# Kernel tuning notes

Hardware: AMD Instinct MI355X
Metric: run time of the kernel (lower is better)

## Reference

```python
import jax, jax.numpy as jnp
import numpy as np

B, C, N, M = 16, 256, 4096, 1024
EPS = 1e-5


def geometry_disentangle(x, num_select):
    # x: [B, C, N]. Variation score = L2 norm of mean-centered feature per point.
    score = jnp.linalg.norm(x - x.mean(axis=2, keepdims=True), axis=1)  # [B, N]
    _, idx_s = jax.lax.top_k(score, num_select)    # sharp: highest variation
    _, idx_g = jax.lax.top_k(-score, num_select)   # gentle: lowest variation
    sharp = jnp.take_along_axis(x, idx_s[:, None, :], axis=2)   # [B, C, M]
    gentle = jnp.take_along_axis(x, idx_g[:, None, :], axis=2)  # [B, C, M]
    return sharp, gentle


def cross_attention(x, ctx, Wq, bq, Wk, bk, Wv, bv, Wo, bo):
    # x: [B, C, N], ctx: [B, M, C] -> [B, C, N]
    c = x.shape[1]
    q = jnp.einsum('bcn,dc->bdn', x, Wq) + bq[None, :, None]  # conv1x1 on x
    k = jnp.einsum('bmc,dc->bmd', ctx, Wk) + bk
    v = jnp.einsum('bmc,dc->bmd', ctx, Wv) + bv
    scores = jnp.einsum('bdn,bmd->bnm', q, k) / jnp.sqrt(jnp.asarray(c, x.dtype))
    attn = jax.nn.softmax(scores, axis=-1)                     # [B, N, M]
    y = jnp.einsum('bnm,bmd->bdn', attn, v)                    # [B, C, N]
    y = jnp.einsum('bdn,ed->ben', y, Wo) + bo[None, :, None]   # output conv1x1
    return x + y


def conv_bn_relu(h, Wf, bf, gamma, beta):
    # Conv1d(k=1) + BatchNorm1d (training-mode batch stats) + ReLU. h: [B, 2C, N]
    y = jnp.einsum('bcn,dc->bdn', h, Wf) + bf[None, :, None]   # [B, C, N]
    mu = y.mean(axis=(0, 2), keepdims=True)
    var = y.var(axis=(0, 2), keepdims=True)
    y = (y - mu) * jax.lax.rsqrt(var + EPS)
    y = y * gamma[None, :, None] + beta[None, :, None]
    return jax.nn.relu(y)


def setup_inputs() -> dict:
    key = jax.random.key(0)
    ks = jax.random.split(key, 20)
    s = 0.02

    def w(k, shape):
        return (jax.random.normal(k, shape, dtype=jnp.float32) * s)

    inp = {
        'x': jax.random.normal(ks[0], (B, C, N), dtype=jnp.float32),
        'num_select': M,
        # sharp attention params
        'Wq_s': w(ks[1], (C, C)), 'bq_s': jnp.zeros((C,), jnp.float32),
        'Wk_s': w(ks[2], (C, C)), 'bk_s': jnp.zeros((C,), jnp.float32),
        'Wv_s': w(ks[3], (C, C)), 'bv_s': jnp.zeros((C,), jnp.float32),
        'Wo_s': w(ks[4], (C, C)), 'bo_s': jnp.zeros((C,), jnp.float32),
        # gentle attention params
        'Wq_g': w(ks[5], (C, C)), 'bq_g': jnp.zeros((C,), jnp.float32),
        'Wk_g': w(ks[6], (C, C)), 'bk_g': jnp.zeros((C,), jnp.float32),
        'Wv_g': w(ks[7], (C, C)), 'bv_g': jnp.zeros((C,), jnp.float32),
        'Wo_g': w(ks[8], (C, C)), 'bo_g': jnp.zeros((C,), jnp.float32),
        # fuse: Conv1d(2C -> C) + BN
        'Wf': w(ks[9], (C, 2 * C)), 'bf': jnp.zeros((C,), jnp.float32),
        'gamma': jnp.ones((C,), jnp.float32), 'beta': jnp.zeros((C,), jnp.float32),
    }
    return inp


def reference(x, Wq_s, bq_s, Wk_s, bk_s, Wv_s, bv_s, Wo_s, bo_s,
              Wq_g, bq_g, Wk_g, bk_g, Wv_g, bv_g, Wo_g, bo_g,
              Wf, bf, gamma, beta, num_select):
    sharp, gentle = geometry_disentangle(x, num_select)
    y_s = cross_attention(x, sharp.transpose(0, 2, 1), Wq_s, bq_s, Wk_s, bk_s, Wv_s, bv_s, Wo_s, bo_s)
    y_g = cross_attention(x, gentle.transpose(0, 2, 1), Wq_g, bq_g, Wk_g, bk_g, Wv_g, bv_g, Wo_g, bo_g)
    h = jnp.concatenate([y_s, y_g], axis=1)  # [B, 2C, N]
    return conv_bn_relu(h, Wf, bf, gamma, beta)
```

## Files before the change

### kernel.cpp

```cpp
#include <hip/hip_runtime.h>

#define BB 16
#define CC 256
#define NN 4096
#define MM 1024
#define EPSV 1e-5f
#define SCALE (1.0f/16.0f)

#define OFF_MU    0
#define OFF_SCORE 4096
#define OFF_IDX   69632
#define OFF_U     102400
#define OFF_WVZ   167936
#define OFF_WF12  233472
#define OFF_BVZ   299008
#define OFF_BZ    299264
#define OFF_W16   299520
#define OFF_XG    430592
#define OFF_K16   2527744
#define OFF_VT16  4624896
#define OFF_Z     6722048
#define OFF_BN    23499264
#define FIXED_F   23499776

typedef __attribute__((ext_vector_type(8))) short s16x8;
typedef __attribute__((ext_vector_type(4))) float f32x4;

__device__ __forceinline__ unsigned short f2bf(float f) {
    unsigned int u = __float_as_uint(f);
    return (unsigned short)((u + 0x7FFFu + ((u >> 16) & 1u)) >> 16);
}
__device__ __forceinline__ float bf2f(unsigned short h) {
    return __uint_as_float(((unsigned int)h) << 16);
}

__global__ __launch_bounds__(256) void zero_bn_kernel(float* bn) {
    int t = threadIdx.x;
    bn[t] = 0.f; bn[t + CC] = 0.f;
}

__global__ __launch_bounds__(256) void zero_rsum_kernel(float* r) {
    r[blockIdx.x * 256 + threadIdx.x] = 0.f;
}

__global__ __launch_bounds__(256) void mean_kernel(const float* __restrict__ x, float* __restrict__ mu) {
    int c = blockIdx.x, b = blockIdx.y, t = threadIdx.x;
    const float4* p = (const float4*)(x + ((size_t)b * CC + c) * NN);
    float s = 0.f;
    for (int n = t; n < NN / 4; n += 256) { float4 v = p[n]; s += (v.x + v.y) + (v.z + v.w); }
    __shared__ float red[256];
    red[t] = s; __syncthreads();
    for (int w = 128; w > 0; w >>= 1) { if (t < w) red[t] += red[t + w]; __syncthreads(); }
    if (t == 0) mu[b * CC + c] = red[0] * (1.0f / NN);
}

__global__ __launch_bounds__(256) void transpose_score_kernel(const float* __restrict__ x,
                                                              const float* __restrict__ mu,
                                                              unsigned short* __restrict__ xT,
                                                              float* __restrict__ score) {
    __shared__ float tile[32][33];
    __shared__ float smu[32];
    int b = blockIdx.z, c0 = blockIdx.y * 32, n0 = blockIdx.x * 32, t = threadIdx.x;
    int nl = t & 31, cr = t >> 5;
    if (t < 32) smu[t] = mu[b * CC + c0 + t];
#pragma unroll
    for (int q = 0; q < 4; ++q)
        tile[cr + q * 8][nl] = x[((size_t)b * CC + c0 + cr + q * 8) * NN + n0 + nl];
    __syncthreads();
    int nr = t >> 3, cq = t & 7;
    uint2 p;
    p.x = (unsigned int)f2bf(tile[cq * 4 + 0][nr]) | ((unsigned int)f2bf(tile[cq * 4 + 1][nr]) << 16);
    p.y = (unsigned int)f2bf(tile[cq * 4 + 2][nr]) | ((unsigned int)f2bf(tile[cq * 4 + 3][nr]) << 16);
    *(uint2*)&xT[((size_t)b * NN + n0 + nr) * CC + c0 + cq * 4] = p;
    int n = t & 31, cseg = t >> 5;
    float part = 0.f;
#pragma unroll
    for (int q = 0; q < 4; ++q) {
        float d = tile[cseg * 4 + q][n] - smu[cseg * 4 + q];
        part += d * d;
    }
    __syncthreads();
    tile[n][cseg] = part;
    __syncthreads();
    if (t < 32) {
        float s = 0.f;
#pragma unroll
        for (int j = 0; j < 8; ++j) s += tile[t][j];
        atomicAdd(&score[(size_t)b * NN + n0 + t], s);
    }
}

__global__ __launch_bounds__(1024) void select_kernel(const float* __restrict__ score,
                                                      int* __restrict__ idx_s, int* __restrict__ idx_g) {
    int b = blockIdx.x, t = threadIdx.x;
    __shared__ unsigned int keys[NN];
    __shared__ unsigned int hist[256];
    __shared__ unsigned int sbin, skrem;
    __shared__ int outcnt, eqcnt;
    __shared__ int eqidx[NN];
    for (int q = t; q < NN; q += 1024) keys[q] = __float_as_uint(score[(size_t)b * NN + q]);
    __syncthreads();
    for (int r = 0; r < 2; ++r) {
        unsigned int flip = r ? 0xFFFFFFFFu : 0u;
        unsigned int prefix = 0u, pmask = 0u;
        unsigned int k = MM;
        for (int pass = 0; pass < 4; ++pass) {
            int shift = 24 - 8 * pass;
            if (t < 256) hist[t] = 0u;
            __syncthreads();
            for (int q = t; q < NN; q += 1024) {
                unsigned int kv = keys[q] ^ flip;
                if ((kv & pmask) == prefix) atomicAdd(&hist[(kv >> shift) & 255u], 1u);
            }
            __syncthreads();
            for (int off = 1; off < 256; off <<= 1) {
                unsigned int v = 0u;
                if (t < 256) v = hist[t] + ((t + off < 256) ? hist[t + off] : 0u);
                __syncthreads();
                if (t < 256) hist[t] = v;
                __syncthreads();
            }
            if (t < 256) {
                unsigned int sj = hist[t], sj1 = (t < 255) ? hist[t + 1] : 0u;
                if (sj >= k && sj1 < k) { sbin = (unsigned int)t; skrem = k - sj1; }
            }
            __syncthreads();
            prefix |= sbin << shift;
            pmask |= 0xFFu << shift;
            k = skrem;
            __syncthreads();
        }
        unsigned int T = prefix;
        unsigned int krem = k;
        int* outp = r ? idx_g : idx_s;
        if (t == 0) { outcnt = 0; eqcnt = 0; }
        __syncthreads();
        for (int q = t; q < NN; q += 1024) {
            unsigned int kv = keys[q] ^ flip;
            if (kv > T) { int pp = atomicAdd(&outcnt, 1); outp[(size_t)b * MM + pp] = q; }
            else if (kv == T) { int pp = atomicAdd(&eqcnt, 1); eqidx[pp] = q; }
        }
        __syncthreads();
        int ne = eqcnt;
        for (int i = t; i < ne; i += 1024) {
            int me = eqidx[i];
            int rank = 0;
            for (int j = 0; j < ne; ++j) rank += (eqidx[j] < me) ? 1 : 0;
            if (rank < (int)krem) { int pp = atomicAdd(&outcnt, 1); outp[(size_t)b * MM + pp] = me; }
        }
        __syncthreads();
    }
}

__global__ __launch_bounds__(256) void bz_kernel(const float* __restrict__ Wf, const float* __restrict__ bf,
                                                 const float* __restrict__ bo_s, const float* __restrict__ bo_g,
                                                 float* __restrict__ bz) {
    int e = threadIdx.x;
    float acc = bf[e];
    for (int c = 0; c < CC; ++c)
        acc += Wf[e * 2 * CC + c] * bo_s[c] + Wf[e * 2 * CC + CC + c] * bo_g[c];
    bz[e] = acc;
}

__global__ __launch_bounds__(256) void wf12_kernel(const float* __restrict__ Wf, float* __restrict__ Wf12) {
    int e = blockIdx.x, c = threadIdx.x;
    Wf12[e * CC + c] = Wf[e * 2 * CC + c] + Wf[e * 2 * CC + CC + c];
}

__global__ __launch_bounds__(256) void prep1_kernel(
    const float* __restrict__ Wo, const float* __restrict__ Wv,
    const float* __restrict__ Wq, const float* __restrict__ Wk,
    const float* __restrict__ bq, const float* __restrict__ bk, const float* __restrict__ bv,
    float* __restrict__ WoWv, unsigned short* __restrict__ W2_16,
    float* __restrict__ wob, float* __restrict__ u, float* __restrict__ b2)
{
    int xr = blockIdx.x, y = blockIdx.y, t = threadIdx.x;
    if (y == 0) {
        __shared__ float arow[CC];
        arow[t] = Wo[xr * CC + t];
        __syncthreads();
        float acc = 0.f;
        for (int k = 0; k < CC; ++k) acc += arow[k] * Wv[k * CC + t];
        WoWv[xr * CC + t] = acc;
    } else if (y == 1) {
        __shared__ float aq[CC];
        aq[t] = Wq[t * CC + xr];
        __syncthreads();
        float acc = 0.f;
        for (int c = 0; c < CC; ++c) acc += aq[c] * Wk[c * CC + t];
        W2_16[xr * CC + t] = f2bf(acc);
    } else if (xr == 0) {
        float a1 = 0.f, a2 = 0.f, a3 = 0.f;
        for (int c = 0; c < CC; ++c) {
            a1 += Wo[t * CC + c] * bv[c];
            a2 += bq[c] * Wk[c * CC + t];
            a3 += Wq[c * CC + t] * bk[c];
        }
        wob[t] = a1; u[t] = a2; b2[t] = a3;
        if (t == 0) { float s = 0.f; for (int c = 0; c < CC; ++c) s += bq[c] * bk[c]; u[CC] = s; }
    }
}

__global__ __launch_bounds__(256) void prep2_kernel(
    const float* __restrict__ Wf, int aoff, const float* __restrict__ WoWv,
    const float* __restrict__ wob, unsigned short* __restrict__ Wvz16, float* __restrict__ bvz)
{
    int e = blockIdx.x, t = threadIdx.x;
    __shared__ float arow[CC];
    __shared__ float red[256];
    arow[t] = Wf[e * 2 * CC + aoff + t];
    __syncthreads();
    float acc = 0.f;
    for (int k = 0; k < CC; ++k) acc += arow[k] * WoWv[k * CC + t];
    Wvz16[e * CC + t] = f2bf(acc);
    red[t] = arow[t] * wob[t];
    __syncthreads();
    for (int w = 128; w > 0; w >>= 1) { if (t < w) red[t] += red[t + w]; __syncthreads(); }
    if (t == 0) bvz[e] = red[0];
}

__global__ __launch_bounds__(256) void beta_kernel(const unsigned short* __restrict__ Xg,
                                                   const float* __restrict__ u, float* __restrict__ beta) {
    int row = blockIdx.x * 4 + (threadIdx.x >> 6);
    int l = threadIdx.x & 63;
    uint2 p = *(const uint2*)&Xg[(size_t)row * CC + l * 4];
    float acc = bf2f((unsigned short)(p.x & 0xFFFF)) * u[l * 4]
              + bf2f((unsigned short)(p.x >> 16)) * u[l * 4 + 1]
              + bf2f((unsigned short)(p.y & 0xFFFF)) * u[l * 4 + 2]
              + bf2f((unsigned short)(p.y >> 16)) * u[l * 4 + 3];
    acc += __shfl_xor(acc, 1); acc += __shfl_xor(acc, 2); acc += __shfl_xor(acc, 4);
    acc += __shfl_xor(acc, 8); acc += __shfl_xor(acc, 16); acc += __shfl_xor(acc, 32);
    if (l == 0) beta[row] = acc + u[CC];
}

__global__ __launch_bounds__(256) void conv_bf16_kernel(const float* __restrict__ src,
                                                        unsigned short* __restrict__ dst) {
    int i = blockIdx.x * 256 + threadIdx.x;
    float4 v = *(const float4*)(src + (size_t)i * 4);
    uint2 p;
    p.x = (unsigned int)f2bf(v.x) | ((unsigned int)f2bf(v.y) << 16);
    p.y = (unsigned int)f2bf(v.z) | ((unsigned int)f2bf(v.w) << 16);
    *(uint2*)&dst[(size_t)i * 4] = p;
}

__global__ __launch_bounds__(256) void gather_kernel(const unsigned short* __restrict__ xT,
                                                     const int* __restrict__ idx,
                                                     unsigned short* __restrict__ Xg) {
    int row = blockIdx.x * 4 + (threadIdx.x >> 6);
    int l = threadIdx.x & 63;
    int b = row >> 10, m = row & (MM - 1);
    int src = idx[b * MM + m];
    *(uint2*)&Xg[(size_t)row * CC + l * 4] =
        *(const uint2*)&xT[((size_t)b * NN + src) * CC + l * 4];
}

template<int OMODE>
__global__ __launch_bounds__(256, 3) void gemm_bt(
    const unsigned short* __restrict__ A, size_t a_bs,
    const unsigned short* __restrict__ Bw, size_t b_bs,
    const float* __restrict__ bias,
    void* __restrict__ outp, size_t o_bs, int ldo)
{
    __shared__ __align__(16) unsigned short As[128 * 32];
    __shared__ __align__(16) unsigned short Bs[128 * 32];
    int z = blockIdx.z;
    const unsigned short* Ab = A + z * a_bs + (size_t)blockIdx.x * 128 * CC;
    const unsigned short* Bb = Bw + z * b_bs + (size_t)blockIdx.y * 128 * CC;
    int t = threadIdx.x, w = t >> 6, l = t & 63, g = l >> 4, c16 = l & 15;
    int wi = w >> 1, wj = w & 1;
    int srow = t >> 2, skq = (t & 3) * 8;

    f32x4 acc[4][4];
#pragma unroll
    for (int a = 0; a < 4; ++a)
#pragma unroll
        for (int bq = 0; bq < 4; ++bq) acc[a][bq] = (f32x4){0.f, 0.f, 0.f, 0.f};

    for (int ks = 0; ks < 8; ++ks) {
        int k0 = ks * 32;
        uint4 a0 = *(const uint4*)(Ab + (size_t)srow * CC + k0 + skq);
        uint4 a1 = *(const uint4*)(Ab + (size_t)(srow + 64) * CC + k0 + skq);
        uint4 b0 = *(const uint4*)(Bb + (size_t)srow * CC + k0 + skq);
        uint4 b1 = *(const uint4*)(Bb + (size_t)(srow + 64) * CC + k0 + skq);
        __syncthreads();
        *(uint4*)&As[srow * 32 + skq] = a0;
        *(uint4*)&As[(srow + 64) * 32 + skq] = a1;
        *(uint4*)&Bs[srow * 32 + skq] = b0;
        *(uint4*)&Bs[(srow + 64) * 32 + skq] = b1;
        __syncthreads();
        s16x8 af[4], bf4[4];
#pragma unroll
        for (int fi = 0; fi < 4; ++fi)
            af[fi] = *(const s16x8*)&As[(wi * 64 + fi * 16 + c16) * 32 + g * 8];
#pragma unroll
        for (int fj = 0; fj < 4; ++fj)
            bf4[fj] = *(const s16x8*)&Bs[(wj * 64 + fj * 16 + c16) * 32 + g * 8];
#pragma unroll
        for (int fi = 0; fi < 4; ++fi)
#pragma unroll
            for (int fj = 0; fj < 4; ++fj)
                acc[fi][fj] = __builtin_amdgcn_mfma_f32_16x16x32_bf16(af[fi], bf4[fj], acc[fi][fj], 0, 0, 0);
    }

    int i0 = blockIdx.x * 128 + wi * 64, j0 = blockIdx.y * 128 + wj * 64;
#pragma unroll
    for (int fi = 0; fi < 4; ++fi) {
#pragma unroll
        for (int fj = 0; fj < 4; ++fj) {
            int colg = j0 + fj * 16 + c16;
#pragma unroll
            for (int r = 0; r < 4; ++r) {
                int rowg = i0 + fi * 16 + g * 4 + r;
                float v = acc[fi][fj][r] + (OMODE == 2 ? bias[rowg] : bias[colg]);
                if (OMODE == 0)
                    ((float*)outp)[z * o_bs + (size_t)rowg * ldo + colg] = v;
                else
                    ((unsigned short*)outp)[z * o_bs + (size_t)rowg * ldo + colg] = f2bf(v);
            }
        }
    }
}

__global__ __attribute__((amdgpu_flat_work_group_size(512, 512)))
__attribute__((amdgpu_waves_per_eu(2, 2)))
void fused_attn(
    const unsigned short* __restrict__ Q,
    const unsigned short* __restrict__ K,
    const unsigned short* __restrict__ Vt,
    const float* __restrict__ beta,
    float* __restrict__ Z)
{
    extern __shared__ __align__(16) unsigned char smem[];
    float* rsl = (float*)(smem + 114688);
    float* bs  = (float*)(smem + 115712);

    int z = blockIdx.z;
    int n0 = blockIdx.x * 128;
    int t = threadIdx.x, w = t >> 6, l = t & 63, g = l >> 4, c16 = l & 15;
    int wn = w >> 1, wc = w & 1;

    const unsigned short* Qb = Q + ((size_t)z * NN + n0) * CC;
    const char* Kzb = (const char*)(K + (size_t)z * MM * CC);
    const char* Vzb = (const char*)(Vt + (size_t)z * CC * MM);

    bs[t] = beta[(size_t)z * MM + t];
    bs[t + 512] = beta[(size_t)z * MM + t + 512];

    s16x8 q[2][8];
#pragma unroll
    for (int fi = 0; fi < 2; ++fi)
#pragma unroll
        for (int ks = 0; ks < 8; ++ks)
            q[fi][ks] = *(const s16x8*)&Qb[(size_t)(wn * 32 + fi * 16 + c16) * CC + ks * 32 + g * 8];

    f32x4 o[2][8];
#pragma unroll
    for (int fi = 0; fi < 2; ++fi)
#pragma unroll
        for (int fj = 0; fj < 8; ++fj) o[fi][fj] = (f32x4){0.f, 0.f, 0.f, 0.f};
    float rs[2][4];
#pragma unroll
    for (int fi = 0; fi < 2; ++fi)
#pragma unroll
        for (int r = 0; r < 4; ++r) rs[fi][r] = 0.f;

    auto issueK = [&](int buf, int m0) {
#pragma unroll
        for (int j = 0; j < 2; ++j) {
            int cid = w * 2 + j;
            int row = cid * 2 + (l >> 5);
            int srcoff = ((l & 31) * 16) ^ ((row & 7) << 4);
            const char* gp = Kzb + (size_t)(m0 + row) * 512 + srcoff;
            __builtin_amdgcn_global_load_lds(
                (const __attribute__((address_space(1))) void*)gp,
                (__attribute__((address_space(3))) void*)(smem + buf * 16384 + cid * 1024),
                16, 0, 0);
        }
    };
    auto issueV = [&](int slot, int m0) {
#pragma unroll
        for (int j = 0; j < 2; ++j) {
            int cid = w * 2 + j;
            int row = cid * 16 + (l >> 2);
            int srcoff = ((l & 3) * 16) ^ (((row >> 1) & 3) << 4);
            const char* gp = Vzb + (size_t)row * 2048 + (size_t)m0 * 2 + srcoff;
            __builtin_amdgcn_global_load_lds(
                (const __attribute__((address_space(1))) void*)gp,
                (__attribute__((address_space(3))) void*)(smem + 32768 + slot * 16384 + cid * 1024),
                16, 0, 0);
        }
    };

    auto qk_exp = [&](int buf, int par, int m0) {
        const unsigned char* Ks = smem + buf * 16384;
        unsigned char* Ps = smem + 81920 + par * 16384;
        f32x4 sacc[2];
#pragma unroll
        for (int fi = 0; fi < 2; ++fi) sacc[fi] = (f32x4){0.f, 0.f, 0.f, 0.f};
        int mr = wc * 16 + c16;
        __builtin_amdgcn_s_setprio(1);
#pragma unroll
        for (int ks = 0; ks < 8; ++ks) {
            s16x8 kf = *(const s16x8*)(Ks + ((mr * 512 + ks * 64 + g * 16) ^ ((mr & 7) << 4)));
#pragma unroll
            for (int fi = 0; fi < 2; ++fi)
                sacc[fi] = __builtin_amdgcn_mfma_f32_16x16x32_bf16(q[fi][ks], kf, sacc[fi], 0, 0, 0);
        }
        __builtin_amdgcn_s_setprio(0);
        float bet = bs[m0 + wc * 16 + c16];
#pragma unroll
        for (int fi = 0; fi < 2; ++fi)
#pragma unroll
            for (int r = 0; r < 4; ++r) {
                float e = __expf((sacc[fi][r] + bet) * SCALE);
                unsigned short h = f2bf(e);
                int nr = wn * 32 + fi * 16 + g * 4 + r;
                *(unsigned short*)(Ps + ((nr * 128 + (wc * 16 + c16) * 2) ^ ((nr & 7) << 4))) = h;
                rs[fi][r] += bf2f(h);
            }
    };
    auto pv = [&](int slot, int par) {
        const unsigned char* Vs = smem + 32768 + slot * 16384;
        const unsigned char* Ps = smem + 81920 + par * 16384;
        s16x8 pa[2];
#pragma unroll
        for (int fi = 0; fi < 2; ++fi) {
            int nr = wn * 32 + fi * 16 + c16;
            pa[fi] = *(const s16x8*)(Ps + ((nr * 128 + g * 16) ^ ((nr & 7) << 4)));
        }
        __builtin_amdgcn_s_setprio(1);
#pragma unroll
        for (int fj = 0; fj < 8; ++fj) {
            int er = wc * 128 + fj * 16 + c16;
            s16x8 vb = *(const s16x8*)(Vs + ((er * 64 + g * 16) ^ (((er >> 1) & 3) << 4)));
#pragma unroll
            for (int fi = 0; fi < 2; ++fi)
                o[fi][fj] = __builtin_amdgcn_mfma_f32_16x16x32_bf16(pa[fi], vb, o[fi][fj], 0, 0, 0);
        }
        __builtin_amdgcn_s_setprio(0);
    };

    issueK(0, 0); issueV(0, 0);
    issueK(1, 32); issueV(1, 32);
    __syncthreads();
    qk_exp(0, 0, 0);

    for (int mt = 0; mt < 32; ++mt) {
        __syncthreads();
        if (mt < 30) {
            issueK(mt & 1, (mt + 2) * 32);
            issueV((mt + 2) % 3, (mt + 2) * 32);
        }
        __builtin_amdgcn_sched_barrier(0);
        if (mt < 31) qk_exp((mt + 1) & 1, (mt + 1) & 1, (mt + 1) * 32);
        pv(mt % 3, mt & 1);
    }

#pragma unroll
    for (int fi = 0; fi < 2; ++fi)
#pragma unroll
        for (int r = 0; r < 4; ++r) {
            float v = rs[fi][r];
            v += __shfl_xor(v, 1); v += __shfl_xor(v, 2);
            v += __shfl_xor(v, 4); v += __shfl_xor(v, 8);
            if (c16 == 0) rsl[wc * 128 + wn * 32 + fi * 16 + g * 4 + r] = v;
        }
    __syncthreads();
    float* Zb = Z + ((size_t)z * NN + n0) * CC;
#pragma unroll
    for (int fi = 0; fi < 2; ++fi)
#pragma unroll
        for (int r = 0; r < 4; ++r) {
            int nr = wn * 32 + fi * 16 + g * 4 + r;
            float inv = 1.0f / (rsl[nr] + rsl[128 + nr]);
#pragma unroll
            for (int fj = 0; fj < 8; ++fj) {
                int e = wc * 128 + fj * 16 + c16;
                Zb[(size_t)nr * CC + e] += o[fi][fj][r] * inv;
            }
        }
}

__global__ __launch_bounds__(256) void bn_stats_kernel(const float* __restrict__ Z, float* __restrict__ bn) {
    int blk = blockIdx.x, e = threadIdx.x;
    const float* p = Z + (size_t)blk * 256 * CC + e;
    float s1 = 0.f, s2 = 0.f;
    for (int r = 0; r < 256; ++r) { float v = p[(size_t)r * CC]; s1 += v; s2 += v * v; }
    atomicAdd(&bn[e], s1);
    atomicAdd(&bn[CC + e], s2);
}

__global__ __launch_bounds__(256) void bn_apply_kernel(const float* __restrict__ Z, const float* __restrict__ bn,
                                                       const float* __restrict__ gamma, const float* __restrict__ beta,
                                                       float* __restrict__ out) {
    int b = blockIdx.z, e0 = blockIdx.y * 32, n0 = blockIdx.x * 32, t = threadIdx.x;
    __shared__ float tile[32][33];
    int c = t & 31, r0 = (t >> 5) * 4;
#pragma unroll
    for (int q = 0; q < 4; ++q)
        tile[r0 + q][c] = Z[((size_t)b * NN + n0 + r0 + q) * CC + e0 + c];
    __syncthreads();
    int n = t & 31, er0 = (t >> 5) * 4;
    const float invcnt = 1.0f / (BB * NN);
#pragma unroll
    for (int q = 0; q < 4; ++q) {
        int e = e0 + er0 + q;
        float mean = bn[e] * invcnt;
        float var = bn[CC + e] * invcnt - mean * mean;
        float rsq = rsqrtf(var + EPSV);
        float v = (tile[n][er0 + q] - mean) * rsq * gamma[e] + beta[e];
        out[((size_t)b * CC + e) * NN + n0 + n] = fmaxf(v, 0.f);
    }
}

extern "C" void kernel_launch(void* const* d_in, const int* in_sizes, int n_in,
                              void* d_out, int out_size, void* d_ws, size_t ws_size,
                              hipStream_t stream) {
    const float* x    = (const float*)d_in[0];
    const float* Wq_s = (const float*)d_in[2];  const float* bq_s = (const float*)d_in[3];
    const float* Wk_s = (const float*)d_in[4];  const float* bk_s = (const float*)d_in[5];
    const float* Wv_s = (const float*)d_in[6];  const float* bv_s = (const float*)d_in[7];
    const float* Wo_s = (const float*)d_in[8];  const float* bo_s = (const float*)d_in[9];
    const float* Wq_g = (const float*)d_in[10]; const float* bq_g = (const float*)d_in[11];
    const float* Wk_g = (const float*)d_in[12]; const float* bk_g = (const float*)d_in[13];
    const float* Wv_g = (const float*)d_in[14]; const float* bv_g = (const float*)d_in[15];
    const float* Wo_g = (const float*)d_in[16]; const float* bo_g = (const float*)d_in[17];
    const float* Wf   = (const float*)d_in[18]; const float* bf   = (const float*)d_in[19];
    const float* gamma = (const float*)d_in[20]; const float* beta = (const float*)d_in[21];

    float* ws    = (float*)d_ws;
    float* mu    = ws + OFF_MU;
    float* score = ws + OFF_SCORE;
    int*   idx_s = (int*)(ws + OFF_IDX);
    int*   idx_g = idx_s + BB * MM;
    float* WoWv  = ws + OFF_U;
    float* Wf12  = ws + OFF_WF12;
    float* bvz   = ws + OFF_BVZ;
    float* bz    = ws + OFF_BZ;
    float* uvec  = ws + OFF_MU;
    float* b2    = ws + OFF_MU + 512;
    float* wob   = ws + OFF_MU + 1024;
    float* betaA = ws + OFF_SCORE;
    unsigned short* Wf12_16 = (unsigned short*)(ws + OFF_W16);
    unsigned short* W2_16   = Wf12_16 + 65536;
    unsigned short* Wvz16   = W2_16 + 65536;
    unsigned short* Xg16 = (unsigned short*)(ws + OFF_XG);
    unsigned short* K16  = (unsigned short*)(ws + OFF_K16);
    unsigned short* Vt16 = (unsigned short*)(ws + OFF_VT16);
    float* Z     = ws + OFF_Z;
    float* bn    = ws + OFF_BN;
    unsigned short* xT16 = (unsigned short*)d_out + (size_t)BB * NN * CC;

    zero_bn_kernel<<<1, 256, 0, stream>>>(bn);
    mean_kernel<<<dim3(CC, BB), 256, 0, stream>>>(x, mu);
    zero_rsum_kernel<<<BB * NN / 256, 256, 0, stream>>>(score);
    transpose_score_kernel<<<dim3(NN / 32, CC / 32, BB), 256, 0, stream>>>(x, mu, xT16, score);
    select_kernel<<<BB, 1024, 0, stream>>>(score, idx_s, idx_g);
    wf12_kernel<<<CC, 256, 0, stream>>>(Wf, Wf12);
    bz_kernel<<<1, 256, 0, stream>>>(Wf, bf, bo_s, bo_g, bz);
    conv_bf16_kernel<<<64, 256, 0, stream>>>(Wf12, Wf12_16);
    gemm_bt<0><<<dim3(512, 2, 1), 256, 0, stream>>>(xT16, 0, Wf12_16, 0, bz, Z, 0, CC);

    for (int br = 0; br < 2; ++br) {
        const float* Wo = br ? Wo_g : Wo_s;
        const float* Wv = br ? Wv_g : Wv_s;  const float* bv = br ? bv_g : bv_s;
        const float* Wk = br ? Wk_g : Wk_s;  const float* bk = br ? bk_g : bk_s;
        const float* Wq = br ? Wq_g : Wq_s;  const float* bq = br ? bq_g : bq_s;
        int* idx = br ? idx_g : idx_s;
        int aoff = br ? CC : 0;
        prep1_kernel<<<dim3(CC, 3), 256, 0, stream>>>(Wo, Wv, Wq, Wk, bq, bk, bv,
                                                      WoWv, W2_16, wob, uvec, b2);
        prep2_kernel<<<CC, 256, 0, stream>>>(Wf, aoff, WoWv, wob, Wvz16, bvz);
        gather_kernel<<<BB * MM / 4, 256, 0, stream>>>(xT16, idx, Xg16);
        gemm_bt<1><<<dim3(BB * MM / 128, 2, 1), 256, 0, stream>>>(Xg16, 0, W2_16, 0, b2, K16, 0, CC);
        beta_kernel<<<BB * MM / 4, 256, 0, stream>>>(Xg16, uvec, betaA);
        gemm_bt<2><<<dim3(2, 8, BB), 256, 0, stream>>>(Wvz16, 0, Xg16, (size_t)MM * CC, bvz,
                                                       Vt16, (size_t)CC * MM, MM);

        fused_attn<<<dim3(NN / 128, 1, BB), 512, 119808, stream>>>(xT16, K16, Vt16, betaA, Z);
    }

    bn_stats_kernel<<<BB * NN / 256, 256, 0, stream>>>(Z, bn);
    bn_apply_kernel<<<dim3(NN / 32, CC / 32, BB), 256, 0, stream>>>(Z, bn, gamma, beta, (float*)d_out);
}
```

Measured before the change: 593.7 us.

## Fuse both attention branches and BN statistics into one attention kernel

The two per-branch fused_attn launches become a single launch that loops over both branches inside each block, keeping the sharp branch's normalized output in registers. The Z read-modify-write then happens once instead of twice, and the BatchNorm sum and sum-of-squares are reduced in LDS and added atomically to global memory, which removes the separate bn_stats pass over Z. The gentle branch's K/V buffers move into spare space in the output buffer so both branches stay live. The extra oS register array (64 floats) raises register pressure in a kernel pinned to 2 waves per EU and may cause spills.

```diff
diff --git a/kernel.cpp b/kernel.cpp
--- a/kernel.cpp
+++ b/kernel.cpp
@@ -11,7 +11,6 @@
 #define OFF_SCORE 4096
 #define OFF_IDX   69632
 #define OFF_U     102400
-#define OFF_WVZ   167936
 #define OFF_WF12  233472
 #define OFF_BVZ   299008
 #define OFF_BZ    299264
@@ -21,7 +20,6 @@
 #define OFF_VT16  4624896
 #define OFF_Z     6722048
 #define OFF_BN    23499264
-#define FIXED_F   23499776
 
 typedef __attribute__((ext_vector_type(8))) short s16x8;
 typedef __attribute__((ext_vector_type(4))) float f32x4;
@@ -325,14 +323,19 @@
 __attribute__((amdgpu_waves_per_eu(2, 2)))
 void fused_attn(
     const unsigned short* __restrict__ Q,
-    const unsigned short* __restrict__ K,
-    const unsigned short* __restrict__ Vt,
-    const float* __restrict__ beta,
-    float* __restrict__ Z)
+    const unsigned short* __restrict__ Ks_,
+    const unsigned short* __restrict__ Vs_,
+    const float* __restrict__ betas_,
+    const unsigned short* __restrict__ Kg_,
+    const unsigned short* __restrict__ Vg_,
+    const float* __restrict__ betag_,
+    float* __restrict__ Z,
+    float* __restrict__ bn)
 {
     extern __shared__ __align__(16) unsigned char smem[];
     float* rsl = (float*)(smem + 114688);
     float* bs  = (float*)(smem + 115712);
+    float* stats = (float*)(smem + 81920);
 
     int z = blockIdx.z;
     int n0 = blockIdx.x * 128;
@@ -340,11 +343,7 @@
     int wn = w >> 1, wc = w & 1;
 
     const unsigned short* Qb = Q + ((size_t)z * NN + n0) * CC;
-    const char* Kzb = (const char*)(K + (size_t)z * MM * CC);
-    const char* Vzb = (const char*)(Vt + (size_t)z * CC * MM);
-
-    bs[t] = beta[(size_t)z * MM + t];
-    bs[t + 512] = beta[(size_t)z * MM + t + 512];
+    const char* Kcur; const char* Vcur;
 
     s16x8 q[2][8];
 #pragma unroll
@@ -353,16 +352,9 @@
         for (int ks = 0; ks < 8; ++ks)
             q[fi][ks] = *(const s16x8*)&Qb[(size_t)(wn * 32 + fi * 16 + c16) * CC + ks * 32 + g * 8];
 
+    f32x4 oS[2][8];
     f32x4 o[2][8];
-#pragma unroll
-    for (int fi = 0; fi < 2; ++fi)
-#pragma unroll
-        for (int fj = 0; fj < 8; ++fj) o[fi][fj] = (f32x4){0.f, 0.f, 0.f, 0.f};
     float rs[2][4];
-#pragma unroll
-    for (int fi = 0; fi < 2; ++fi)
-#pragma unroll
-        for (int r = 0; r < 4; ++r) rs[fi][r] = 0.f;
 
     auto issueK = [&](int buf, int m0) {
 #pragma unroll
@@ -370,7 +362,7 @@
             int cid = w * 2 + j;
             int row = cid * 2 + (l >> 5);
             int srcoff = ((l & 31) * 16) ^ ((row & 7) << 4);
-            const char* gp = Kzb + (size_t)(m0 + row) * 512 + srcoff;
+            const char* gp = Kcur + (size_t)(m0 + row) * 512 + srcoff;
             __builtin_amdgcn_global_load_lds(
                 (const __attribute__((address_space(1))) void*)gp,
                 (__attribute__((address_space(3))) void*)(smem + buf * 16384 + cid * 1024),
@@ -383,7 +375,7 @@
             int cid = w * 2 + j;
             int row = cid * 16 + (l >> 2);
             int srcoff = ((l & 3) * 16) ^ (((row >> 1) & 3) << 4);
-            const char* gp = Vzb + (size_t)row * 2048 + (size_t)m0 * 2 + srcoff;
+            const char* gp = Vcur + (size_t)row * 2048 + (size_t)m0 * 2 + srcoff;
             __builtin_amdgcn_global_load_lds(
                 (const __attribute__((address_space(1))) void*)gp,
                 (__attribute__((address_space(3))) void*)(smem + 32768 + slot * 16384 + cid * 1024),
@@ -440,54 +432,90 @@
         __builtin_amdgcn_s_setprio(0);
     };
 
-    issueK(0, 0); issueV(0, 0);
-    issueK(1, 32); issueV(1, 32);
-    __syncthreads();
-    qk_exp(0, 0, 0);
-
-    for (int mt = 0; mt < 32; ++mt) {
-        __syncthreads();
-        if (mt < 30) {
-            issueK(mt & 1, (mt + 2) * 32);
-            issueV((mt + 2) % 3, (mt + 2) * 32);
-        }
-        __builtin_amdgcn_sched_barrier(0);
-        if (mt < 31) qk_exp((mt + 1) & 1, (mt + 1) & 1, (mt + 1) * 32);
-        pv(mt % 3, mt & 1);
-    }
-
-#pragma unroll
-    for (int fi = 0; fi < 2; ++fi)
-#pragma unroll
-        for (int r = 0; r < 4; ++r) {
-            float v = rs[fi][r];
-            v += __shfl_xor(v, 1); v += __shfl_xor(v, 2);
-            v += __shfl_xor(v, 4); v += __shfl_xor(v, 8);
-            if (c16 == 0) rsl[wc * 128 + wn * 32 + fi * 16 + g * 4 + r] = v;
-        }
+    for (int br = 0; br < 2; ++br) {
+        Kcur = (const char*)((br ? Kg_ : Ks_) + (size_t)z * MM * CC);
+        Vcur = (const char*)((br ? Vg_ : Vs_) + (size_t)z * CC * MM);
+        const float* beta = br ? betag_ : betas_;
+        __syncthreads();
+        bs[t] = beta[(size_t)z * MM + t];
+        bs[t + 512] = beta[(size_t)z * MM + t + 512];
+#pragma unroll
+        for (int fi = 0; fi < 2; ++fi) {
+#pragma unroll
+            for (int fj = 0; fj < 8; ++fj) o[fi][fj] = (f32x4){0.f, 0.f, 0.f, 0.f};
+#pragma unroll
+            for (int r = 0; r < 4; ++r) rs[fi][r] = 0.f;
+        }
+        issueK(0, 0); issueV(0, 0);
+        issueK(1, 32); issueV(1, 32);
+        __syncthreads();
+        qk_exp(0, 0, 0);
+        for (int mt = 0; mt < 32; ++mt) {
+            __syncthreads();
+            if (mt < 30) {
+                issueK(mt & 1, (mt + 2) * 32);
+                issueV((mt + 2) % 3, (mt + 2) * 32);
+            }
+            __builtin_amdgcn_sched_barrier(0);
+            if (mt < 31) qk_exp((mt + 1) & 1, (mt + 1) & 1, (mt + 1) * 32);
+            pv(mt % 3, mt & 1);
+        }
+#pragma unroll
+        for (int fi = 0; fi < 2; ++fi)
+#pragma unroll
+            for (int r = 0; r < 4; ++r) {
+                float v = rs[fi][r];
+                v += __shfl_xor(v, 1); v += __shfl_xor(v, 2);
+                v += __shfl_xor(v, 4); v += __shfl_xor(v, 8);
+                if (c16 == 0) rsl[wc * 128 + wn * 32 + fi * 16 + g * 4 + r] = v;
+            }
+        __syncthreads();
+#pragma unroll
+        for (int fi = 0; fi < 2; ++fi)
+#pragma unroll
+            for (int r = 0; r < 4; ++r) {
+                int nr = wn * 32 + fi * 16 + g * 4 + r;
+                float inv = 1.0f / (rsl[nr] + rsl[128 + nr]);
+#pragma unroll
+                for (int fj = 0; fj < 8; ++fj) {
+                    if (br == 0) oS[fi][fj][r] = o[fi][fj][r] * inv;
+                    else         o[fi][fj][r] *= inv;
+                }
+            }
+    }
+
+    __syncthreads();
+    stats[t] = 0.f;
     __syncthreads();
     float* Zb = Z + ((size_t)z * NN + n0) * CC;
+    float s1p[8], s2p[8];
+#pragma unroll
+    for (int fj = 0; fj < 8; ++fj) { s1p[fj] = 0.f; s2p[fj] = 0.f; }
 #pragma unroll
     for (int fi = 0; fi < 2; ++fi)
 #pragma unroll
         for (int r = 0; r < 4; ++r) {
             int nr = wn * 32 + fi * 16 + g * 4 + r;
-            float inv = 1.0f / (rsl[nr] + rsl[128 + nr]);
 #pragma unroll
             for (int fj = 0; fj < 8; ++fj) {
                 int e = wc * 128 + fj * 16 + c16;
-                Zb[(size_t)nr * CC + e] += o[fi][fj][r] * inv;
-            }
-        }
-}
-
-__global__ __launch_bounds__(256) void bn_stats_kernel(const float* __restrict__ Z, float* __restrict__ bn) {
-    int blk = blockIdx.x, e = threadIdx.x;
-    const float* p = Z + (size_t)blk * 256 * CC + e;
-    float s1 = 0.f, s2 = 0.f;
-    for (int r = 0; r < 256; ++r) { float v = p[(size_t)r * CC]; s1 += v; s2 += v * v; }
-    atomicAdd(&bn[e], s1);
-    atomicAdd(&bn[CC + e], s2);
+                float fv = Zb[(size_t)nr * CC + e] + oS[fi][fj][r] + o[fi][fj][r];
+                Zb[(size_t)nr * CC + e] = fv;
+                s1p[fj] += fv;
+                s2p[fj] += fv * fv;
+            }
+        }
+#pragma unroll
+    for (int fj = 0; fj < 8; ++fj) {
+        int e = wc * 128 + fj * 16 + c16;
+        atomicAdd(&stats[e], s1p[fj]);
+        atomicAdd(&stats[256 + e], s2p[fj]);
+    }
+    __syncthreads();
+    if (t < 256) {
+        atomicAdd(&bn[t], stats[t]);
+        atomicAdd(&bn[CC + t], stats[256 + t]);
+    }
 }
 
 __global__ __launch_bounds__(256) void bn_apply_kernel(const float* __restrict__ Z, const float* __restrict__ bn,
@@ -540,16 +568,19 @@
     float* uvec  = ws + OFF_MU;
     float* b2    = ws + OFF_MU + 512;
     float* wob   = ws + OFF_MU + 1024;
-    float* betaA = ws + OFF_SCORE;
+    float* betaS = ws + OFF_SCORE;
+    float* betaG = ws + OFF_SCORE + BB * MM;
     unsigned short* Wf12_16 = (unsigned short*)(ws + OFF_W16);
     unsigned short* W2_16   = Wf12_16 + 65536;
     unsigned short* Wvz16   = W2_16 + 65536;
     unsigned short* Xg16 = (unsigned short*)(ws + OFF_XG);
-    unsigned short* K16  = (unsigned short*)(ws + OFF_K16);
-    unsigned short* Vt16 = (unsigned short*)(ws + OFF_VT16);
+    unsigned short* K16s = (unsigned short*)(ws + OFF_K16);
+    unsigned short* Vt16s = (unsigned short*)(ws + OFF_VT16);
     float* Z     = ws + OFF_Z;
     float* bn    = ws + OFF_BN;
-    unsigned short* xT16 = (unsigned short*)d_out + (size_t)BB * NN * CC;
+    unsigned short* K16g  = (unsigned short*)d_out;
+    unsigned short* Vt16g = K16g + (size_t)BB * MM * CC;
+    unsigned short* xT16  = (unsigned short*)d_out + (size_t)BB * NN * CC;
 
     zero_bn_kernel<<<1, 256, 0, stream>>>(bn);
     mean_kernel<<<dim3(CC, BB), 256, 0, stream>>>(x, mu);
@@ -568,6 +599,9 @@
         const float* Wq = br ? Wq_g : Wq_s;  const float* bq = br ? bq_g : bq_s;
         int* idx = br ? idx_g : idx_s;
         int aoff = br ? CC : 0;
+        unsigned short* K16  = br ? K16g : K16s;
+        unsigned short* Vt16 = br ? Vt16g : Vt16s;
+        float* betaA = br ? betaG : betaS;
         prep1_kernel<<<dim3(CC, 3), 256, 0, stream>>>(Wo, Wv, Wq, Wk, bq, bk, bv,
                                                       WoWv, W2_16, wob, uvec, b2);
         prep2_kernel<<<CC, 256, 0, stream>>>(Wf, aoff, WoWv, wob, Wvz16, bvz);
@@ -576,10 +610,10 @@
         beta_kernel<<<BB * MM / 4, 256, 0, stream>>>(Xg16, uvec, betaA);
         gemm_bt<2><<<dim3(2, 8, BB), 256, 0, stream>>>(Wvz16, 0, Xg16, (size_t)MM * CC, bvz,
                                                        Vt16, (size_t)CC * MM, MM);
-
-        fused_attn<<<dim3(NN / 128, 1, BB), 512, 119808, stream>>>(xT16, K16, Vt16, betaA, Z);
-    }
-
-    bn_stats_kernel<<<BB * NN / 256, 256, 0, stream>>>(Z, bn);
+    }
+
+    fused_attn<<<dim3(NN / 128, 1, BB), 512, 119808, stream>>>(
+        xT16, K16s, Vt16s, betaS, K16g, Vt16g, betaG, Z, bn);
+
     bn_apply_kernel<<<dim3(NN / 32, CC / 32, BB), 256, 0, stream>>>(Z, bn, gamma, beta, (float*)d_out);
 }
```

Measured after the change: 639.1 us. +7.6%, slower.

## Fuse channel-mean computation into transpose pass via sum-of-squares score expansion

Applied to the files above, without the earlier changes.

Drops the separate mean kernel that read all of x a second time. The transpose kernel now accumulates per-point sum of squares and per-channel sums with atomics. A new score_fix kernel then subtracts the cross term (2/N)·x·sum_x, using the bf16 transposed copy of x. The per-batch constant ||mu||^2 is omitted, which is safe because it does not change the top-k ordering. This saves one full fp32 read of x, but adds a bf16 read and an extra launch, and the expanded form can lose precision through cancellation.

```diff
diff --git a/kernel.cpp b/kernel.cpp
--- a/kernel.cpp
+++ b/kernel.cpp
@@ -11,7 +11,6 @@
 #define OFF_SCORE 4096
 #define OFF_IDX   69632
 #define OFF_U     102400
-#define OFF_WVZ   167936
 #define OFF_WF12  233472
 #define OFF_BVZ   299008
 #define OFF_BZ    299264
@@ -21,7 +20,6 @@
 #define OFF_VT16  4624896
 #define OFF_Z     6722048
 #define OFF_BN    23499264
-#define FIXED_F   23499776
 
 typedef __attribute__((ext_vector_type(8))) short s16x8;
 typedef __attribute__((ext_vector_type(4))) float f32x4;
@@ -43,26 +41,13 @@
     r[blockIdx.x * 256 + threadIdx.x] = 0.f;
 }
 
-__global__ __launch_bounds__(256) void mean_kernel(const float* __restrict__ x, float* __restrict__ mu) {
-    int c = blockIdx.x, b = blockIdx.y, t = threadIdx.x;
-    const float4* p = (const float4*)(x + ((size_t)b * CC + c) * NN);
-    float s = 0.f;
-    for (int n = t; n < NN / 4; n += 256) { float4 v = p[n]; s += (v.x + v.y) + (v.z + v.w); }
-    __shared__ float red[256];
-    red[t] = s; __syncthreads();
-    for (int w = 128; w > 0; w >>= 1) { if (t < w) red[t] += red[t + w]; __syncthreads(); }
-    if (t == 0) mu[b * CC + c] = red[0] * (1.0f / NN);
-}
-
-__global__ __launch_bounds__(256) void transpose_score_kernel(const float* __restrict__ x,
-                                                              const float* __restrict__ mu,
-                                                              unsigned short* __restrict__ xT,
-                                                              float* __restrict__ score) {
+__global__ __launch_bounds__(256) void transpose_s2_kernel(const float* __restrict__ x,
+                                                           unsigned short* __restrict__ xT,
+                                                           float* __restrict__ score,
+                                                           float* __restrict__ musum) {
     __shared__ float tile[32][33];
-    __shared__ float smu[32];
     int b = blockIdx.z, c0 = blockIdx.y * 32, n0 = blockIdx.x * 32, t = threadIdx.x;
     int nl = t & 31, cr = t >> 5;
-    if (t < 32) smu[t] = mu[b * CC + c0 + t];
 #pragma unroll
     for (int q = 0; q < 4; ++q)
         tile[cr + q * 8][nl] = x[((size_t)b * CC + c0 + cr + q * 8) * NN + n0 + nl];
@@ -72,22 +57,47 @@
     p.x = (unsigned int)f2bf(tile[cq * 4 + 0][nr]) | ((unsigned int)f2bf(tile[cq * 4 + 1][nr]) << 16);
     p.y = (unsigned int)f2bf(tile[cq * 4 + 2][nr]) | ((unsigned int)f2bf(tile[cq * 4 + 3][nr]) << 16);
     *(uint2*)&xT[((size_t)b * NN + n0 + nr) * CC + c0 + cq * 4] = p;
-    int n = t & 31, cseg = t >> 5;
-    float part = 0.f;
+    int a = t & 31, seg = t >> 5;
+    float ps2 = 0.f, pmu = 0.f;
 #pragma unroll
     for (int q = 0; q < 4; ++q) {
-        float d = tile[cseg * 4 + q][n] - smu[cseg * 4 + q];
-        part += d * d;
-    }
-    __syncthreads();
-    tile[n][cseg] = part;
+        float v = tile[seg * 4 + q][a];
+        ps2 += v * v;
+        pmu += tile[a][seg * 4 + q];
+    }
+    __syncthreads();
+    tile[a][seg] = ps2;
+    tile[a][8 + seg] = pmu;
     __syncthreads();
     if (t < 32) {
         float s = 0.f;
 #pragma unroll
         for (int j = 0; j < 8; ++j) s += tile[t][j];
         atomicAdd(&score[(size_t)b * NN + n0 + t], s);
-    }
+    } else if (t < 64) {
+        int r = t - 32;
+        float s = 0.f;
+#pragma unroll
+        for (int j = 0; j < 8; ++j) s += tile[r][8 + j];
+        atomicAdd(&musum[b * CC + c0 + r], s);
+    }
+}
+
+__global__ __launch_bounds__(256) void score_fix_kernel(const unsigned short* __restrict__ xT,
+                                                        const float* __restrict__ musum,
+                                                        float* __restrict__ score) {
+    int row = blockIdx.x * 4 + (threadIdx.x >> 6);
+    int l = threadIdx.x & 63;
+    int b = row >> 12;
+    uint2 p = *(const uint2*)&xT[(size_t)row * CC + l * 4];
+    const float* ms = musum + b * CC + l * 4;
+    float acc = bf2f((unsigned short)(p.x & 0xFFFF)) * ms[0]
+              + bf2f((unsigned short)(p.x >> 16)) * ms[1]
+              + bf2f((unsigned short)(p.y & 0xFFFF)) * ms[2]
+              + bf2f((unsigned short)(p.y >> 16)) * ms[3];
+    acc += __shfl_xor(acc, 1); acc += __shfl_xor(acc, 2); acc += __shfl_xor(acc, 4);
+    acc += __shfl_xor(acc, 8); acc += __shfl_xor(acc, 16); acc += __shfl_xor(acc, 32);
+    if (l == 0) score[row] -= acc * (2.0f / NN);
 }
 
 __global__ __launch_bounds__(1024) void select_kernel(const float* __restrict__ score,
@@ -529,7 +539,7 @@
     const float* gamma = (const float*)d_in[20]; const float* beta = (const float*)d_in[21];
 
     float* ws    = (float*)d_ws;
-    float* mu    = ws + OFF_MU;
+    float* musum = ws + OFF_MU;
     float* score = ws + OFF_SCORE;
     int*   idx_s = (int*)(ws + OFF_IDX);
     int*   idx_g = idx_s + BB * MM;
@@ -552,9 +562,9 @@
     unsigned short* xT16 = (unsigned short*)d_out + (size_t)BB * NN * CC;
 
     zero_bn_kernel<<<1, 256, 0, stream>>>(bn);
-    mean_kernel<<<dim3(CC, BB), 256, 0, stream>>>(x, mu);
-    zero_rsum_kernel<<<BB * NN / 256, 256, 0, stream>>>(score);
-    transpose_score_kernel<<<dim3(NN / 32, CC / 32, BB), 256, 0, stream>>>(x, mu, xT16, score);
+    zero_rsum_kernel<<<272, 256, 0, stream>>>(ws);
+    transpose_s2_kernel<<<dim3(NN / 32, CC / 32, BB), 256, 0, stream>>>(x, xT16, score, musum);
+    score_fix_kernel<<<BB * NN / 4, 256, 0, stream>>>(xT16, musum, score);
     select_kernel<<<BB, 1024, 0, stream>>>(score, idx_s, idx_g);
     wf12_kernel<<<CC, 256, 0, stream>>>(Wf, Wf12);
     bz_kernel<<<1, 256, 0, stream>>>(Wf, bf, bo_s, bo_g, bz);
```

New measurement: 599.0 us. No clear change (+0.9%).
